# Performance work log

Hardware: AMD Instinct MI355X
Metric: run time of the kernel (lower is better)

Reference implementation:

```python
import jax, jax.numpy as jnp
import numpy as np

B, L, D, H, DH, M = 2, 2048, 512, 8, 2048, 128  # batch, seq, d_model, heads, d_hidden, max_rel_pos
HD = D // H
EPS = 1e-5


def _ln(x, w, b):
    mu = jnp.mean(x, axis=-1, keepdims=True)
    var = jnp.mean((x - mu) ** 2, axis=-1, keepdims=True)
    return (x - mu) * jax.lax.rsqrt(var + EPS) * w + b


def setup_inputs() -> dict:
    key = jax.random.key(0)
    ks = jax.random.split(key, 8)
    s = 0.02  # init std for weights
    return {
        "x": jax.random.normal(ks[0], (B, L, D), jnp.float32),
        "ln1_w": jnp.ones((D,), jnp.float32),
        "ln1_b": jnp.zeros((D,), jnp.float32),
        "qkv_w": jax.random.normal(ks[1], (D, 3 * D), jnp.float32) * s,
        "qkv_b": jnp.zeros((3 * D,), jnp.float32),
        "out_w": jax.random.normal(ks[2], (D, D), jnp.float32) * s,
        "out_b": jnp.zeros((D,), jnp.float32),
        "rel_bias": jax.random.normal(ks[3], (H, 2 * M - 1), jnp.float32) * s,
        "gamma1": 1e-4 * jnp.ones((D,), jnp.float32),
        "ln2_w": jnp.ones((D,), jnp.float32),
        "ln2_b": jnp.zeros((D,), jnp.float32),
        "ffn_in_w": jax.random.normal(ks[4], (D, 2 * DH), jnp.float32) * s,
        "ffn_in_b": jnp.zeros((2 * DH,), jnp.float32),
        "ffn_out_w": jax.random.normal(ks[5], (DH, D), jnp.float32) * s,
        "ffn_out_b": jnp.zeros((D,), jnp.float32),
        "gamma2": 1e-4 * jnp.ones((D,), jnp.float32),
    }


def _forward(x, ln1_w, ln1_b, qkv_w, qkv_b, out_w, out_b, rel_bias, gamma1,
             ln2_w, ln2_b, ffn_in_w, ffn_in_b, ffn_out_w, ffn_out_b, gamma2):
    b, l, d = x.shape
    # --- PreNorm attention with T5-style relative position bias ---
    h = _ln(x, ln1_w, ln1_b)
    qkv = h @ qkv_w + qkv_b                           # [B, L, 3D]
    q, k, v = jnp.split(qkv, 3, axis=-1)
    q = q.reshape(b, l, H, HD)
    k = k.reshape(b, l, H, HD)
    v = v.reshape(b, l, H, HD)
    scale = 1.0 / jnp.sqrt(jnp.asarray(HD, x.dtype))
    scores = jnp.einsum("bqhd,bkhd->bhqk", q, k) * scale   # [B, H, L, L]
    # relative position bias: clip(i - j) indexed into learned table
    ctx = jnp.arange(l)[:, None] - jnp.arange(l)[None, :]
    ctx = jnp.clip(ctx, -(M - 1), M - 1) + (M - 1)          # [L, L] in [0, 2M-2]
    rel = rel_bias[:, ctx]                                  # [H, L, L]
    scores = scores + rel[None]
    attn = jax.nn.softmax(scores, axis=-1)
    o = jnp.einsum("bhqk,bkhd->bqhd", attn, v).reshape(b, l, d)
    o = o @ out_w + out_b
    x = x + o * gamma1                                      # LayerScale residual
    # --- PreNorm GEGLU FFN ---
    h2 = _ln(x, ln2_w, ln2_b)
    ab = h2 @ ffn_in_w + ffn_in_b                           # [B, L, 2*DH]
    a, bgate = jnp.split(ab, 2, axis=-1)
    f = jax.nn.gelu(bgate, approximate=False) * a
    f = f @ ffn_out_w + ffn_out_b
    x = x + f * gamma2
    return x, attn


def reference(x, ln1_w, ln1_b, qkv_w, qkv_b, out_w, out_b, rel_bias, gamma1,
              ln2_w, ln2_b, ffn_in_w, ffn_in_b, ffn_out_w, ffn_out_b, gamma2):
    return _forward(x, ln1_w, ln1_b, qkv_w, qkv_b, out_w, out_b, rel_bias, gamma1,
                    ln2_w, ln2_b, ffn_in_w, ffn_in_b, ffn_out_w, ffn_out_b, gamma2)
```

## Files before the change

### kernel.cpp

```cpp
#include <hip/hip_runtime.h>
#include <math.h>

typedef __attribute__((ext_vector_type(4))) float f32x4;
typedef __attribute__((ext_vector_type(8))) short bf16x8;
typedef __attribute__((ext_vector_type(4))) short s16x4;

#if __has_builtin(__builtin_amdgcn_exp2f)
#define EXP2(x) __builtin_amdgcn_exp2f(x)
#else
#define EXP2(x) exp2f(x)
#endif

__device__ __forceinline__ unsigned short f2bf(float f) {
  union { float f; unsigned u; } v; v.f = f;
  return (unsigned short)((v.u + 0x7fffu + ((v.u >> 16) & 1u)) >> 16);
}

__global__ void ln_kernel(const float* __restrict__ in, const float* __restrict__ w,
                          const float* __restrict__ b, unsigned short* __restrict__ out) {
  __shared__ float sh[4];
  const int t = threadIdx.x;
  const float* p = in + (size_t)blockIdx.x * 512;
  float a0 = p[t], a1 = p[t + 256];
  float s = a0 + a1;
#pragma unroll
  for (int o = 32; o; o >>= 1) s += __shfl_down(s, o);
  if ((t & 63) == 0) sh[t >> 6] = s;
  __syncthreads();
  s = sh[0] + sh[1] + sh[2] + sh[3];
  float mu = s * (1.0f / 512.0f);
  float d0 = a0 - mu, d1 = a1 - mu;
  float q = d0 * d0 + d1 * d1;
  __syncthreads();
#pragma unroll
  for (int o = 32; o; o >>= 1) q += __shfl_down(q, o);
  if ((t & 63) == 0) sh[t >> 6] = q;
  __syncthreads();
  q = sh[0] + sh[1] + sh[2] + sh[3];
  float rstd = rsqrtf(q * (1.0f / 512.0f) + 1e-5f);
  unsigned short* po = out + (size_t)blockIdx.x * 512;
  po[t]       = f2bf(d0 * rstd * w[t] + b[t]);
  po[t + 256] = f2bf(d1 * rstd * w[t + 256] + b[t + 256]);
}

__global__ void transpose_all(const float* __restrict__ w0, unsigned short* __restrict__ o0,
                              const float* __restrict__ w1, unsigned short* __restrict__ o1,
                              const float* __restrict__ w2, unsigned short* __restrict__ o2,
                              const float* __restrict__ w3, unsigned short* __restrict__ o3) {
  __shared__ float tile[32][33];
  int idx = blockIdx.x;
  const float* in; unsigned short* out; int ldi, ldo, nx;
  if (idx < 768)        { in = w0; out = o0; ldi = 1536; ldo = 512;  nx = 48; }
  else if (idx < 1024)  { idx -= 768;  in = w1; out = o1; ldi = 512;  ldo = 512;  nx = 16; }
  else if (idx < 3072)  { idx -= 1024; in = w2; out = o2; ldi = 4096; ldo = 512;  nx = 128; }
  else                  { idx -= 3072; in = w3; out = o3; ldi = 512;  ldo = 2048; nx = 16; }
  const int tx = threadIdx.x & 31;
  const int ty = threadIdx.x >> 5;
  const int n0 = (idx % nx) * 32, k0 = (idx / nx) * 32;
#pragma unroll
  for (int i = 0; i < 4; ++i)
    tile[ty + i * 8][tx] = in[(size_t)(k0 + ty + i * 8) * ldi + n0 + tx];
  __syncthreads();
#pragma unroll
  for (int i = 0; i < 4; ++i)
    out[(size_t)(n0 + ty + i * 8) * ldo + k0 + tx] = f2bf(tile[tx][ty + i * 8]);
}

template <int WM, int WN, int TM, int TN, int EPI>
__global__ __launch_bounds__(256) void gemm_bb(
    const unsigned short* __restrict__ A, const unsigned short* __restrict__ Bt,
    float* __restrict__ C, unsigned short* __restrict__ Cbf, unsigned short* __restrict__ Vt,
    int K, int lda, int ldb, int ldc,
    const float* __restrict__ bias, const float* __restrict__ resid,
    const float* __restrict__ gamma) {
  constexpr int BM = WM * TM * 16;
  constexpr int BN = WN * TN * 16;
  constexpr int LDS_STRIDE = 72;
  __shared__ short As[BM * LDS_STRIDE];
  __shared__ short Bs[BN * LDS_STRIDE];

  const int tid = threadIdx.x;
  const int m0 = blockIdx.y * BM, n0 = blockIdx.x * BN;
  const int w = tid >> 6, lane = tid & 63;
  const int wm = w / WN, wn = w % WN;
  const int lrow = lane & 15, lq = lane >> 4;

  f32x4 acc[TM][TN];
#pragma unroll
  for (int i = 0; i < TM; ++i)
#pragma unroll
    for (int j = 0; j < TN; ++j) acc[i][j] = (f32x4){0.f, 0.f, 0.f, 0.f};

  for (int k0 = 0; k0 < K; k0 += 64) {
    __syncthreads();
#pragma unroll
    for (int it = 0; it < BM / 32; ++it) {
      int c = it * 256 + tid;
      int row = c >> 3, col = (c & 7) << 3;
      *(bf16x8*)(As + row * LDS_STRIDE + col) =
          *(const bf16x8*)(A + (size_t)(m0 + row) * lda + k0 + col);
    }
#pragma unroll
    for (int it = 0; it < BN / 32; ++it) {
      int c = it * 256 + tid;
      int row = c >> 3, col = (c & 7) << 3;
      *(bf16x8*)(Bs + row * LDS_STRIDE + col) =
          *(const bf16x8*)(Bt + (size_t)(n0 + row) * ldb + k0 + col);
    }
    __syncthreads();

    bf16x8 af[TM][2], bf[TN][2];
#pragma unroll
    for (int mi = 0; mi < TM; ++mi)
#pragma unroll
      for (int c = 0; c < 2; ++c)
        af[mi][c] = *(const bf16x8*)(As + (wm * TM * 16 + mi * 16 + lrow) * LDS_STRIDE + c * 32 + lq * 8);
#pragma unroll
    for (int nj = 0; nj < TN; ++nj)
#pragma unroll
      for (int c = 0; c < 2; ++c)
        bf[nj][c] = *(const bf16x8*)(Bs + (wn * TN * 16 + nj * 16 + lrow) * LDS_STRIDE + c * 32 + lq * 8);
#pragma unroll
    for (int mi = 0; mi < TM; ++mi)
#pragma unroll
      for (int nj = 0; nj < TN; ++nj)
#pragma unroll
        for (int c = 0; c < 2; ++c)
          acc[mi][nj] = __builtin_amdgcn_mfma_f32_16x16x32_bf16(af[mi][c], bf[nj][c], acc[mi][nj], 0, 0, 0);
  }

#pragma unroll
  for (int mi = 0; mi < TM; ++mi) {
#pragma unroll
    for (int nj = 0; nj < TN; ++nj) {
      int gm0 = m0 + wm * TM * 16 + mi * 16 + lq * 4;
      int gn = n0 + wn * TN * 16 + nj * 16 + lrow;
      if constexpr (EPI == 4) {
        if (gn >= 1024) {
          int h = (gn - 1024) >> 6, dd = (gn - 1024) & 63;
          int bb = gm0 >> 11, l0 = gm0 & 2047;
          float bs = bias[gn];
          s16x4 r4 = {(short)f2bf(acc[mi][nj][0] + bs), (short)f2bf(acc[mi][nj][1] + bs),
                      (short)f2bf(acc[mi][nj][2] + bs), (short)f2bf(acc[mi][nj][3] + bs)};
          *(s16x4*)(Vt + ((size_t)(bb * 8 + h) * 64 + dd) * 2048 + l0) = r4;
          continue;
        }
      }
#pragma unroll
      for (int r = 0; r < 4; ++r) {
        int gm = gm0 + r;
        size_t idx = (size_t)gm * ldc + gn;
        float v = acc[mi][nj][r];
        if constexpr (EPI == 0) {
          C[idx] = v + bias[gn];
        } else if constexpr (EPI == 4) {
          float u = v + bias[gn];
          Cbf[idx] = f2bf(gn < 512 ? u * 0.18033688011112042f : u);
        } else {
          C[idx] = resid[idx] + (v + bias[gn]) * gamma[gn];
        }
      }
    }
  }
}

__global__ __launch_bounds__(256) void ffn1_gate_kernel(
    const unsigned short* __restrict__ A, const unsigned short* __restrict__ Bt,
    unsigned short* __restrict__ F, const float* __restrict__ bias) {
  constexpr int LDS_STRIDE = 72;
  __shared__ short As[128 * LDS_STRIDE];
  __shared__ short Bs[64 * LDS_STRIDE];
  __shared__ short Bs2[64 * LDS_STRIDE];

  const int tid = threadIdx.x;
  const int n0 = blockIdx.x * 64, m0 = blockIdx.y * 128;
  const int w = tid >> 6, lane = tid & 63;
  const int wm = w >> 1, wn = w & 1;
  const int lrow = lane & 15, lq = lane >> 4;

  f32x4 acca[4][2], accb[4][2];
#pragma unroll
  for (int i = 0; i < 4; ++i)
#pragma unroll
    for (int j = 0; j < 2; ++j) {
      acca[i][j] = (f32x4){0.f, 0.f, 0.f, 0.f};
      accb[i][j] = (f32x4){0.f, 0.f, 0.f, 0.f};
    }

  for (int k0 = 0; k0 < 512; k0 += 64) {
    __syncthreads();
#pragma unroll
    for (int it = 0; it < 4; ++it) {
      int c = it * 256 + tid;
      int row = c >> 3, col = (c & 7) << 3;
      *(bf16x8*)(As + row * LDS_STRIDE + col) =
          *(const bf16x8*)(A + (size_t)(m0 + row) * 512 + k0 + col);
    }
#pragma unroll
    for (int it = 0; it < 2; ++it) {
      int c = it * 256 + tid;
      int row = c >> 3, col = (c & 7) << 3;
      *(bf16x8*)(Bs + row * LDS_STRIDE + col) =
          *(const bf16x8*)(Bt + (size_t)(n0 + row) * 512 + k0 + col);
      *(bf16x8*)(Bs2 + row * LDS_STRIDE + col) =
          *(const bf16x8*)(Bt + (size_t)(2048 + n0 + row) * 512 + k0 + col);
    }
    __syncthreads();

    bf16x8 af[4][2], ba[2][2], bb[2][2];
#pragma unroll
    for (int mi = 0; mi < 4; ++mi)
#pragma unroll
      for (int c = 0; c < 2; ++c)
        af[mi][c] = *(const bf16x8*)(As + (wm * 64 + mi * 16 + lrow) * LDS_STRIDE + c * 32 + lq * 8);
#pragma unroll
    for (int nj = 0; nj < 2; ++nj)
#pragma unroll
      for (int c = 0; c < 2; ++c) {
        ba[nj][c] = *(const bf16x8*)(Bs + (wn * 32 + nj * 16 + lrow) * LDS_STRIDE + c * 32 + lq * 8);
        bb[nj][c] = *(const bf16x8*)(Bs2 + (wn * 32 + nj * 16 + lrow) * LDS_STRIDE + c * 32 + lq * 8);
      }
#pragma unroll
    for (int mi = 0; mi < 4; ++mi)
#pragma unroll
      for (int nj = 0; nj < 2; ++nj)
#pragma unroll
        for (int c = 0; c < 2; ++c) {
          acca[mi][nj] = __builtin_amdgcn_mfma_f32_16x16x32_bf16(af[mi][c], ba[nj][c], acca[mi][nj], 0, 0, 0);
          accb[mi][nj] = __builtin_amdgcn_mfma_f32_16x16x32_bf16(af[mi][c], bb[nj][c], accb[mi][nj], 0, 0, 0);
        }
  }

#pragma unroll
  for (int mi = 0; mi < 4; ++mi)
#pragma unroll
    for (int nj = 0; nj < 2; ++nj) {
      int gm0 = m0 + wm * 64 + mi * 16 + lq * 4;
      int gn = n0 + wn * 32 + nj * 16 + lrow;
#pragma unroll
      for (int r = 0; r < 4; ++r) {
        float a = acca[mi][nj][r] + bias[gn];
        float bg = accb[mi][nj][r] + bias[2048 + gn];
        float g = 0.5f * bg * (1.0f + erff(bg * 0.70710678118654752f));
        F[(size_t)(gm0 + r) * 2048 + gn] = f2bf(g * a);
      }
    }
}

__global__ __launch_bounds__(256, 4) void attn_fused(
    const unsigned short* __restrict__ qkvbf, const unsigned short* __restrict__ vt,
    const float* __restrict__ rel, float* __restrict__ attn, unsigned short* __restrict__ o) {
  __shared__ __align__(16) float p_f32[4 * 16 * 64];
  __shared__ float erel[256];
  __shared__ float rsum[32];
  __shared__ float rinv[32];

  const int tid = threadIdx.x;
  const int flat = blockIdx.y * 64 + blockIdx.x;
  const int swz = (flat & 7) * 128 + (flat >> 3);
  const int bh = swz >> 6;
  const int m0 = (swz & 63) * 32;
  const int b = bh >> 3, h = bh & 7;

  const int w = tid >> 6, lane = tid & 63;
  const int wm = w >> 1, wn = w & 1;
  const int lrow = lane & 15, lq = lane >> 4;

  const unsigned short* qb = qkvbf + (size_t)(b * 2048) * 1536 + h * 64;
  const unsigned short* kb = qb + 512;
  const unsigned short* vb = vt + (size_t)bh * 64 * 2048;
  float* ab = attn + (size_t)bh * 2048 * 2048;
  const float* relh = rel + h * 255;

  if (tid < 32) rsum[tid] = 0.f;
  if (tid < 255) erel[tid] = __expf(relh[tid]);

  bf16x8 qf[2];
#pragma unroll
  for (int c = 0; c < 2; ++c)
    qf[c] = *(const bf16x8*)(qb + (size_t)(m0 + wm * 16 + lrow) * 1536 + c * 32 + lq * 8);

  const unsigned short* krow = kb + (size_t)(wn * 64 + lrow) * 1536 + lq * 8;
  const unsigned short* vrow = vb + (size_t)lrow * 2048 + wn * 64 + lq * 8;

  __syncthreads();

  float psum[4] = {0.f, 0.f, 0.f, 0.f};
  const int dbase = (m0 + wm * 16 + lq * 4) - (wn * 64 + lrow);
  for (int t = 0; t < 16; ++t) {
    const int kt0 = t * 128;
    f32x4 acc[4];
#pragma unroll
    for (int nj = 0; nj < 4; ++nj) acc[nj] = (f32x4){0.f, 0.f, 0.f, 0.f};
#pragma unroll
    for (int c = 0; c < 2; ++c) {
      bf16x8 kf[4];
#pragma unroll
      for (int nj = 0; nj < 4; ++nj)
        kf[nj] = *(const bf16x8*)(krow + (size_t)(kt0 + nj * 16) * 1536 + c * 32);
#pragma unroll
      for (int nj = 0; nj < 4; ++nj)
        acc[nj] = __builtin_amdgcn_mfma_f32_16x16x32_bf16(qf[c], kf[nj], acc[nj], 0, 0, 0);
    }
    const int Dt = m0 - kt0;
    if (Dt >= 256 || Dt <= -160) {
      float ec = erel[Dt >= 256 ? 254 : 0];
#pragma unroll
      for (int r = 0; r < 4; ++r) {
        float s = 0.f;
#pragma unroll
        for (int nj = 0; nj < 4; ++nj) s += EXP2(acc[nj][r]);
        psum[r] += ec * s;
      }
    } else {
#pragma unroll
      for (int nj = 0; nj < 4; ++nj) {
        int d0 = dbase - kt0 - nj * 16;
#pragma unroll
        for (int r = 0; r < 4; ++r) {
          int d = d0 + r;
          d = d < -127 ? -127 : (d > 127 ? 127 : d);
          psum[r] += EXP2(acc[nj][r]) * erel[d + 127];
        }
      }
    }
  }
#pragma unroll
  for (int off = 1; off < 16; off <<= 1)
#pragma unroll
    for (int r = 0; r < 4; ++r) psum[r] += __shfl_xor(psum[r], off);
  if (lrow == 0) {
#pragma unroll
    for (int r = 0; r < 4; ++r) atomicAdd(&rsum[wm * 16 + lq * 4 + r], psum[r]);
  }
  __syncthreads();
  if (tid < 32) rinv[tid] = 1.0f / rsum[tid];
  __syncthreads();
  float rv[4];
#pragma unroll
  for (int r = 0; r < 4; ++r) rv[r] = rinv[wm * 16 + lq * 4 + r];

  f32x4 oacc[4];
#pragma unroll
  for (int nj = 0; nj < 4; ++nj) oacc[nj] = (f32x4){0.f, 0.f, 0.f, 0.f};
  float* pw = p_f32 + w * (16 * 64);

  const int wsw = lq << 4;
  const int rsw = ((lrow >> 2) & 3) << 4;

  for (int t = 0; t < 16; ++t) {
    const int kt0 = t * 128;
    f32x4 acc[4];
#pragma unroll
    for (int nj = 0; nj < 4; ++nj) acc[nj] = (f32x4){0.f, 0.f, 0.f, 0.f};
#pragma unroll
    for (int c = 0; c < 2; ++c) {
      bf16x8 kf[4];
#pragma unroll
      for (int nj = 0; nj < 4; ++nj)
        kf[nj] = *(const bf16x8*)(krow + (size_t)(kt0 + nj * 16) * 1536 + c * 32);
#pragma unroll
      for (int nj = 0; nj < 4; ++nj)
        acc[nj] = __builtin_amdgcn_mfma_f32_16x16x32_bf16(qf[c], kf[nj], acc[nj], 0, 0, 0);
    }

    const int Dt = m0 - kt0;
    if (Dt >= 256 || Dt <= -160) {
      float ec = erel[Dt >= 256 ? 254 : 0];
#pragma unroll
      for (int r = 0; r < 4; ++r) {
        float fr = ec * rv[r];
        int prow = lq * 4 + r;
#pragma unroll
        for (int nj = 0; nj < 4; ++nj) {
          float e = EXP2(acc[nj][r]) * fr;
          pw[prow * 64 + ((nj * 16 + lrow) ^ wsw)] = e;
        }
      }
    } else {
#pragma unroll
      for (int r = 0; r < 4; ++r) {
        int prow = lq * 4 + r;
        int d0 = dbase - kt0 + r;
#pragma unroll
        for (int nj = 0; nj < 4; ++nj) {
          int d = d0 - nj * 16;
          d = d < -127 ? -127 : (d > 127 ? 127 : d);
          float e = EXP2(acc[nj][r]) * (erel[d + 127] * rv[r]);
          pw[prow * 64 + ((nj * 16 + lrow) ^ wsw)] = e;
        }
      }
    }

#pragma unroll
    for (int it = 0; it < 4; ++it) {
      int rr = lq * 4 + it;
      f32x4 vv = *(const f32x4*)(pw + rr * 64 + ((lrow * 4) ^ wsw));
      __builtin_nontemporal_store(
          vv, (f32x4*)(ab + (size_t)(m0 + wm * 16 + rr) * 2048 + kt0 + wn * 64 + lrow * 4));
    }

#pragma unroll
    for (int c2 = 0; c2 < 2; ++c2) {
      const float* pp = pw + lrow * 64 + ((c2 * 32 + lq * 8) ^ rsw);
      f32x4 pa = *(const f32x4*)pp;
      f32x4 pb = *(const f32x4*)(pp + 4);
      bf16x8 ap = {(short)f2bf(pa[0]), (short)f2bf(pa[1]), (short)f2bf(pa[2]), (short)f2bf(pa[3]),
                   (short)f2bf(pb[0]), (short)f2bf(pb[1]), (short)f2bf(pb[2]), (short)f2bf(pb[3])};
      bf16x8 bv[4];
#pragma unroll
      for (int nj = 0; nj < 4; ++nj)
        bv[nj] = *(const bf16x8*)(vrow + (size_t)(nj * 16) * 2048 + kt0 + c2 * 32);
#pragma unroll
      for (int nj = 0; nj < 4; ++nj)
        oacc[nj] = __builtin_amdgcn_mfma_f32_16x16x32_bf16(ap, bv[nj], oacc[nj], 0, 0, 0);
    }
  }

  __syncthreads();
  float* osc = p_f32;
  if (wn == 0) {
#pragma unroll
    for (int nj = 0; nj < 4; ++nj)
#pragma unroll
      for (int r = 0; r < 4; ++r)
        osc[(wm * 16 + lq * 4 + r) * 64 + nj * 16 + lrow] = oacc[nj][r];
  }
  __syncthreads();
  if (wn == 1) {
#pragma unroll
    for (int nj = 0; nj < 4; ++nj)
#pragma unroll
      for (int r = 0; r < 4; ++r) {
        int rr = m0 + wm * 16 + lq * 4 + r;
        float v = oacc[nj][r] + osc[(wm * 16 + lq * 4 + r) * 64 + nj * 16 + lrow];
        o[(size_t)(b * 2048 + rr) * 512 + h * 64 + nj * 16 + lrow] = f2bf(v);
      }
  }
}

extern "C" void kernel_launch(void* const* d_in, const int* in_sizes, int n_in,
                              void* d_out, int out_size, void* d_ws, size_t ws_size,
                              hipStream_t stream) {
  (void)in_sizes; (void)n_in; (void)out_size; (void)ws_size;
  const float* x        = (const float*)d_in[0];
  const float* ln1_w    = (const float*)d_in[1];
  const float* ln1_b    = (const float*)d_in[2];
  const float* qkv_w    = (const float*)d_in[3];
  const float* qkv_b    = (const float*)d_in[4];
  const float* out_w    = (const float*)d_in[5];
  const float* out_b    = (const float*)d_in[6];
  const float* rel_bias = (const float*)d_in[7];
  const float* gamma1   = (const float*)d_in[8];
  const float* ln2_w    = (const float*)d_in[9];
  const float* ln2_b    = (const float*)d_in[10];
  const float* ffn_in_w = (const float*)d_in[11];
  const float* ffn_in_b = (const float*)d_in[12];
  const float* ffn_out_w  = (const float*)d_in[13];
  const float* ffn_out_b  = (const float*)d_in[14];
  const float* gamma2   = (const float*)d_in[15];

  float* x_out = (float*)d_out;
  float* attn  = x_out + (size_t)2 * 2048 * 512;

  float* ws  = (float*)d_ws;
  float* x1  = ws;
  unsigned short* h_bf  = (unsigned short*)(x1 + 2097152);
  unsigned short* o_bf  = h_bf + 2097152;
  unsigned short* f_bf  = o_bf + 2097152;
  unsigned short* qkvbf = f_bf;
  unsigned short* bt_qkv  = f_bf + 8388608;
  unsigned short* bt_out  = bt_qkv + 786432;
  unsigned short* bt_ffn1 = bt_out + 262144;
  unsigned short* bt_ffn2 = bt_ffn1 + 2097152;
  unsigned short* vt      = bt_ffn2 + 1048576;

  transpose_all<<<4096, 256, 0, stream>>>(qkv_w, bt_qkv, out_w, bt_out,
                                          ffn_in_w, bt_ffn1, ffn_out_w, bt_ffn2);

  ln_kernel<<<4096, 256, 0, stream>>>(x, ln1_w, ln1_b, h_bf);

  gemm_bb<2, 2, 4, 2, 4><<<dim3(24, 32, 1), 256, 0, stream>>>(
      h_bf, bt_qkv, nullptr, qkvbf, vt, 512, 512, 512, 1536, qkv_b, nullptr, nullptr);

  attn_fused<<<dim3(64, 16, 1), 256, 0, stream>>>(qkvbf, vt, rel_bias, attn, o_bf);

  gemm_bb<2, 2, 2, 2, 3><<<dim3(8, 64, 1), 256, 0, stream>>>(
      o_bf, bt_out, x1, nullptr, nullptr, 512, 512, 512, 512, out_b, x, gamma1);

  ln_kernel<<<4096, 256, 0, stream>>>(x1, ln2_w, ln2_b, h_bf);

  ffn1_gate_kernel<<<dim3(32, 32, 1), 256, 0, stream>>>(h_bf, bt_ffn1, f_bf, ffn_in_b);

  gemm_bb<2, 2, 2, 2, 3><<<dim3(8, 64, 1), 256, 0, stream>>>(
      f_bf, bt_ffn2, x_out, nullptr, nullptr, 2048, 2048, 2048, 512, ffn_out_b, x1, gamma2);
}
```

Baseline: 536.2 us.

## Use direct global-to-LDS loads with 32-wide K tiles in GEMM kernels

```diff
diff --git a/kernel.cpp b/kernel.cpp
--- a/kernel.cpp
+++ b/kernel.cpp
@@ -14,6 +14,12 @@
 __device__ __forceinline__ unsigned short f2bf(float f) {
   union { float f; unsigned u; } v; v.f = f;
   return (unsigned short)((v.u + 0x7fffu + ((v.u >> 16) & 1u)) >> 16);
+}
+
+__device__ __forceinline__ void gld16(const void* g, void* l) {
+  __builtin_amdgcn_global_load_lds(
+      (const __attribute__((address_space(1))) unsigned int*)g,
+      (__attribute__((address_space(3))) unsigned int*)l, 16, 0, 0);
 }
 
 __global__ void ln_kernel(const float* __restrict__ in, const float* __restrict__ w,
@@ -75,15 +81,15 @@
     const float* __restrict__ gamma) {
   constexpr int BM = WM * TM * 16;
   constexpr int BN = WN * TN * 16;
-  constexpr int LDS_STRIDE = 72;
-  __shared__ short As[BM * LDS_STRIDE];
-  __shared__ short Bs[BN * LDS_STRIDE];
+  __shared__ __align__(16) short As[BM * 32];
+  __shared__ __align__(16) short Bs[BN * 32];
 
   const int tid = threadIdx.x;
   const int m0 = blockIdx.y * BM, n0 = blockIdx.x * BN;
   const int w = tid >> 6, lane = tid & 63;
   const int wm = w / WN, wn = w % WN;
   const int lrow = lane & 15, lq = lane >> 4;
+  const int srow = lane >> 2, scol = (lane & 3) << 3;
 
   f32x4 acc[TM][TN];
 #pragma unroll
@@ -91,42 +97,32 @@
 #pragma unroll
     for (int j = 0; j < TN; ++j) acc[i][j] = (f32x4){0.f, 0.f, 0.f, 0.f};
 
-  for (int k0 = 0; k0 < K; k0 += 64) {
+  for (int k0 = 0; k0 < K; k0 += 32) {
     __syncthreads();
 #pragma unroll
-    for (int it = 0; it < BM / 32; ++it) {
-      int c = it * 256 + tid;
-      int row = c >> 3, col = (c & 7) << 3;
-      *(bf16x8*)(As + row * LDS_STRIDE + col) =
-          *(const bf16x8*)(A + (size_t)(m0 + row) * lda + k0 + col);
-    }
-#pragma unroll
-    for (int it = 0; it < BN / 32; ++it) {
-      int c = it * 256 + tid;
-      int row = c >> 3, col = (c & 7) << 3;
-      *(bf16x8*)(Bs + row * LDS_STRIDE + col) =
-          *(const bf16x8*)(Bt + (size_t)(n0 + row) * ldb + k0 + col);
+    for (int it = 0; it < BM / 64; ++it) {
+      int chunk = it * 4 + w;
+      gld16(A + (size_t)(m0 + chunk * 16 + srow) * lda + k0 + scol, As + chunk * 512);
+    }
+#pragma unroll
+    for (int it = 0; it < BN / 64; ++it) {
+      int chunk = it * 4 + w;
+      gld16(Bt + (size_t)(n0 + chunk * 16 + srow) * ldb + k0 + scol, Bs + chunk * 512);
     }
     __syncthreads();
 
-    bf16x8 af[TM][2], bf[TN][2];
+    bf16x8 af[TM], bf[TN];
 #pragma unroll
     for (int mi = 0; mi < TM; ++mi)
-#pragma unroll
-      for (int c = 0; c < 2; ++c)
-        af[mi][c] = *(const bf16x8*)(As + (wm * TM * 16 + mi * 16 + lrow) * LDS_STRIDE + c * 32 + lq * 8);
+      af[mi] = *(const bf16x8*)(As + (wm * TM * 16 + mi * 16 + lrow) * 32 + lq * 8);
 #pragma unroll
     for (int nj = 0; nj < TN; ++nj)
-#pragma unroll
-      for (int c = 0; c < 2; ++c)
-        bf[nj][c] = *(const bf16x8*)(Bs + (wn * TN * 16 + nj * 16 + lrow) * LDS_STRIDE + c * 32 + lq * 8);
+      bf[nj] = *(const bf16x8*)(Bs + (wn * TN * 16 + nj * 16 + lrow) * 32 + lq * 8);
 #pragma unroll
     for (int mi = 0; mi < TM; ++mi)
 #pragma unroll
       for (int nj = 0; nj < TN; ++nj)
-#pragma unroll
-        for (int c = 0; c < 2; ++c)
-          acc[mi][nj] = __builtin_amdgcn_mfma_f32_16x16x32_bf16(af[mi][c], bf[nj][c], acc[mi][nj], 0, 0, 0);
+        acc[mi][nj] = __builtin_amdgcn_mfma_f32_16x16x32_bf16(af[mi], bf[nj], acc[mi][nj], 0, 0, 0);
   }
 
 #pragma unroll
@@ -167,16 +163,16 @@
 __global__ __launch_bounds__(256) void ffn1_gate_kernel(
     const unsigned short* __restrict__ A, const unsigned short* __restrict__ Bt,
     unsigned short* __restrict__ F, const float* __restrict__ bias) {
-  constexpr int LDS_STRIDE = 72;
-  __shared__ short As[128 * LDS_STRIDE];
-  __shared__ short Bs[64 * LDS_STRIDE];
-  __shared__ short Bs2[64 * LDS_STRIDE];
+  __shared__ __align__(16) short As[128 * 32];
+  __shared__ __align__(16) short Bs[64 * 32];
+  __shared__ __align__(16) short Bs2[64 * 32];
 
   const int tid = threadIdx.x;
   const int n0 = blockIdx.x * 64, m0 = blockIdx.y * 128;
   const int w = tid >> 6, lane = tid & 63;
   const int wm = w >> 1, wn = w & 1;
   const int lrow = lane & 15, lq = lane >> 4;
+  const int srow = lane >> 2, scol = (lane & 3) << 3;
 
   f32x4 acca[4][2], accb[4][2];
 #pragma unroll
@@ -187,48 +183,36 @@
       accb[i][j] = (f32x4){0.f, 0.f, 0.f, 0.f};
     }
 
-  for (int k0 = 0; k0 < 512; k0 += 64) {
+  for (int k0 = 0; k0 < 512; k0 += 32) {
     __syncthreads();
 #pragma unroll
-    for (int it = 0; it < 4; ++it) {
-      int c = it * 256 + tid;
-      int row = c >> 3, col = (c & 7) << 3;
-      *(bf16x8*)(As + row * LDS_STRIDE + col) =
-          *(const bf16x8*)(A + (size_t)(m0 + row) * 512 + k0 + col);
-    }
-#pragma unroll
     for (int it = 0; it < 2; ++it) {
-      int c = it * 256 + tid;
-      int row = c >> 3, col = (c & 7) << 3;
-      *(bf16x8*)(Bs + row * LDS_STRIDE + col) =
-          *(const bf16x8*)(Bt + (size_t)(n0 + row) * 512 + k0 + col);
-      *(bf16x8*)(Bs2 + row * LDS_STRIDE + col) =
-          *(const bf16x8*)(Bt + (size_t)(2048 + n0 + row) * 512 + k0 + col);
+      int chunk = it * 4 + w;
+      gld16(A + (size_t)(m0 + chunk * 16 + srow) * 512 + k0 + scol, As + chunk * 512);
+    }
+    {
+      int chunk = w;
+      gld16(Bt + (size_t)(n0 + chunk * 16 + srow) * 512 + k0 + scol, Bs + chunk * 512);
+      gld16(Bt + (size_t)(2048 + n0 + chunk * 16 + srow) * 512 + k0 + scol, Bs2 + chunk * 512);
     }
     __syncthreads();
 
-    bf16x8 af[4][2], ba[2][2], bb[2][2];
+    bf16x8 af[4], ba[2], bb[2];
 #pragma unroll
     for (int mi = 0; mi < 4; ++mi)
-#pragma unroll
-      for (int c = 0; c < 2; ++c)
-        af[mi][c] = *(const bf16x8*)(As + (wm * 64 + mi * 16 + lrow) * LDS_STRIDE + c * 32 + lq * 8);
-#pragma unroll
-    for (int nj = 0; nj < 2; ++nj)
-#pragma unroll
-      for (int c = 0; c < 2; ++c) {
-        ba[nj][c] = *(const bf16x8*)(Bs + (wn * 32 + nj * 16 + lrow) * LDS_STRIDE + c * 32 + lq * 8);
-        bb[nj][c] = *(const bf16x8*)(Bs2 + (wn * 32 + nj * 16 + lrow) * LDS_STRIDE + c * 32 + lq * 8);
-      }
+      af[mi] = *(const bf16x8*)(As + (wm * 64 + mi * 16 + lrow) * 32 + lq * 8);
+#pragma unroll
+    for (int nj = 0; nj < 2; ++nj) {
+      ba[nj] = *(const bf16x8*)(Bs + (wn * 32 + nj * 16 + lrow) * 32 + lq * 8);
+      bb[nj] = *(const bf16x8*)(Bs2 + (wn * 32 + nj * 16 + lrow) * 32 + lq * 8);
+    }
 #pragma unroll
     for (int mi = 0; mi < 4; ++mi)
 #pragma unroll
-      for (int nj = 0; nj < 2; ++nj)
-#pragma unroll
-        for (int c = 0; c < 2; ++c) {
-          acca[mi][nj] = __builtin_amdgcn_mfma_f32_16x16x32_bf16(af[mi][c], ba[nj][c], acca[mi][nj], 0, 0, 0);
-          accb[mi][nj] = __builtin_amdgcn_mfma_f32_16x16x32_bf16(af[mi][c], bb[nj][c], accb[mi][nj], 0, 0, 0);
-        }
+      for (int nj = 0; nj < 2; ++nj) {
+        acca[mi][nj] = __builtin_amdgcn_mfma_f32_16x16x32_bf16(af[mi], ba[nj], acca[mi][nj], 0, 0, 0);
+        accb[mi][nj] = __builtin_amdgcn_mfma_f32_16x16x32_bf16(af[mi], bb[nj], accb[mi][nj], 0, 0, 0);
+      }
   }
 
 #pragma unroll
```

Result: no change. 540.8 us (+0.9%).
